# Performance work log

Hardware: AMD Instinct MI355X
Metric: run time of the kernel (lower is better)

## Reference

```python
import jax, jax.numpy as jnp
import numpy as np
import math

B, L, CIN = 16, 1024, 14
T = 256            # num_tokens
H = 2 * T          # S4 channel width
N = 32             # S4 state size (d_state)
E = 128            # embedding_dim
DEPTH = 6
BETA0, BETA1 = 1e-4, 2e-2


def conv1x1(W, b, x):
    # W: [O, C], b: [O], x: [B, C, L] -> [B, O, L]
    return jnp.einsum('oc,bcl->bol', W, x) + b[None, :, None]


def layernorm_c(x, g, b):
    # normalize over channel dim of [B, C, L]
    mu = jnp.mean(x, axis=1, keepdims=True)
    var = jnp.mean((x - mu) ** 2, axis=1, keepdims=True)
    return (x - mu) * jax.lax.rsqrt(var + 1e-5) * g[None, :, None] + b[None, :, None]


def s4d(u, log_dt, logA_re, A_im, C_re, C_im, D):
    # Standard S4D: diagonal SSM, ZOH-ish discretization, FFT depthwise conv.
    # u: [B, H, L]
    Lq = u.shape[-1]
    dt = jnp.exp(log_dt)                       # [H]
    A = -jnp.exp(logA_re) + 1j * A_im          # [H, N]
    dtA = A * dt[:, None]                      # [H, N]
    C = (C_re + 1j * C_im) * (jnp.exp(dtA) - 1.0) / A
    V = jnp.exp(dtA[:, :, None] * jnp.arange(Lq, dtype=jnp.float32))  # [H, N, L]
    K = 2.0 * jnp.einsum('hn,hnl->hl', C, V).real                    # [H, L]
    nfft = 2 * Lq
    y = jnp.fft.irfft(jnp.fft.rfft(u, n=nfft) * jnp.fft.rfft(K, n=nfft)[None], n=nfft)[..., :Lq]
    return y + D[None, :, None] * u


def setup_inputs() -> dict:
    key = jax.random.key(0)
    ks = iter(jax.random.split(key, 64))
    nrm = lambda shape, s=1.0: jax.random.normal(next(ks), shape, jnp.float32) * s
    inp = {}
    inp['x'] = nrm((B, L, CIN))
    inp['t'] = jax.random.uniform(next(ks), (B,), jnp.float32, 1e-3, 1.0)
    # diffusion embedding
    inp['gfp_W'] = nrm((E // 2,), 30.0)
    inp['emb_w1'] = nrm((E, E), E ** -0.5); inp['emb_b1'] = jnp.zeros((E,), jnp.float32)
    inp['emb_w2'] = nrm((E, E), E ** -0.5); inp['emb_b2'] = jnp.zeros((E,), jnp.float32)
    # top-level projections
    inp['in_w'] = nrm((T, CIN), CIN ** -0.5); inp['in_b'] = jnp.zeros((T,), jnp.float32)
    inp['out1_w'] = nrm((T, T), T ** -0.5); inp['out1_b'] = jnp.zeros((T,), jnp.float32)
    inp['out2_w'] = nrm((CIN, T), T ** -0.5); inp['out2_b'] = jnp.zeros((CIN,), jnp.float32)
    # per-block params (stacked over depth)
    inp['dp_w'] = nrm((DEPTH, T, E), E ** -0.5); inp['dp_b'] = jnp.zeros((DEPTH, T), jnp.float32)
    inp['ip_w'] = nrm((DEPTH, H, T), T ** -0.5); inp['ip_b'] = jnp.zeros((DEPTH, H), jnp.float32)
    inp['op_w'] = nrm((DEPTH, H, T), T ** -0.5); inp['op_b'] = jnp.zeros((DEPTH, H), jnp.float32)
    # S4D params: [DEPTH, 2, H, ...] (two S4 layers per block)
    lo, hi = math.log(1e-3), math.log(1e-1)
    inp['s4_log_dt'] = jax.random.uniform(next(ks), (DEPTH, 2, H), jnp.float32, lo, hi)
    inp['s4_logA_re'] = jnp.full((DEPTH, 2, H, N), math.log(0.5), jnp.float32)
    inp['s4_A_im'] = jnp.broadcast_to(math.pi * jnp.arange(N, dtype=jnp.float32), (DEPTH, 2, H, N)).copy()
    inp['s4_C_re'] = nrm((DEPTH, 2, H, N), 0.5 ** 0.5)
    inp['s4_C_im'] = nrm((DEPTH, 2, H, N), 0.5 ** 0.5)
    inp['s4_D'] = nrm((DEPTH, 2, H))
    inp['ln_g'] = jnp.ones((DEPTH, 2, H), jnp.float32)
    inp['ln_b'] = jnp.zeros((DEPTH, 2, H), jnp.float32)
    return inp


def reference(x, t, gfp_W, emb_w1, emb_b1, emb_w2, emb_b2, in_w, in_b,
              out1_w, out1_b, out2_w, out2_b, dp_w, dp_b, ip_w, ip_b,
              op_w, op_b, s4_log_dt, s4_logA_re, s4_A_im, s4_C_re, s4_C_im,
              s4_D, ln_g, ln_b):
    xt = jnp.swapaxes(x, -1, -2)  # [B, CIN, L]
    # Gaussian Fourier projection + MLP (SiLU)
    xp = t[:, None] * gfp_W[None, :] * (2.0 * math.pi)
    emb = jnp.concatenate([jnp.sin(xp), jnp.cos(xp)], axis=-1)        # [B, E]
    emb = jax.nn.silu(emb @ emb_w1.T + emb_b1)
    emb = jax.nn.silu(emb @ emb_w2.T + emb_b2)
    h = conv1x1(in_w, in_b, xt)                                       # [B, T, L]
    skip_sum = jnp.zeros_like(h)
    for d in range(DEPTH):
        y = h + (emb @ dp_w[d].T + dp_b[d])[:, :, None]
        y = conv1x1(ip_w[d], ip_b[d], y)                              # [B, H, L]
        y = s4d(y, s4_log_dt[d, 0], s4_logA_re[d, 0], s4_A_im[d, 0], s4_C_re[d, 0], s4_C_im[d, 0], s4_D[d, 0])
        y = layernorm_c(y, ln_g[d, 0], ln_b[d, 0])
        y = s4d(y, s4_log_dt[d, 1], s4_logA_re[d, 1], s4_A_im[d, 1], s4_C_re[d, 1], s4_C_im[d, 1], s4_D[d, 1])
        y = layernorm_c(y, ln_g[d, 1], ln_b[d, 1])
        gate, filt = jnp.split(y, 2, axis=1)
        y = jax.nn.sigmoid(gate) * jnp.tanh(filt)                     # [B, T, L]
        y = conv1x1(op_w[d], op_b[d], y)                              # [B, H, L]
        res, skip = jnp.split(y, 2, axis=1)
        h = (h + res) / math.sqrt(2.0)
        skip_sum = skip_sum + skip
    z = skip_sum / math.sqrt(float(DEPTH))
    z = jax.nn.relu(conv1x1(out1_w, out1_b, z))
    z = conv1x1(out2_w, out2_b, z)                                    # [B, CIN, L]
    beta = BETA0 + t * (BETA1 - BETA0)                                # linear schedule
    z = z / jnp.sqrt(beta)[:, None, None]
    return jnp.swapaxes(z, -1, -2)                                    # [B, L, CIN]
```

## Files before the change

kernel.cpp:

```cpp
#include <hip/hip_runtime.h>

#define BB     16
#define LLEN   1024
#define CINN   14
#define TSZ    256
#define HSZ    512
#define NST    32
#define ESZ    128
#define NDEPTH 6
#define QHN    (HSZ*NST)

#define RS2 0.70710678118654752f
#define IS6 0.40824829046386302f

typedef unsigned short u16;
typedef unsigned int   u32;
typedef _Float16 f16;
typedef __attribute__((ext_vector_type(2)))  _Float16 f16x2;
typedef __attribute__((ext_vector_type(4)))  _Float16 f16x4;
typedef __attribute__((ext_vector_type(8)))  _Float16 f16x8;
typedef __attribute__((ext_vector_type(16))) float    f32x16;

#define OFF_LAM   0u
#define OFF_C     393216u
#define OFF_LAMP  786432u
#define OFF_DPE16 1181696u
#define OFF_Y16   5388288u
#define OFF_HT    9582592u
#define OFF_GT    11679744u
#define OFF_ST    13776896u
#define OFF_ZT    15874048u
#define OFF_MEAN  17971200u
#define OFF_RSTD  17987584u
#define OFF_MATS  18003968u
#define WS_FLOATS 55752704u

#define MATS_PER_LAYER ((size_t)512*12288)

__global__ void consts_kernel(const float* __restrict__ log_dt, const float* __restrict__ logA,
                              const float* __restrict__ Aim,   const float* __restrict__ Cre,
                              const float* __restrict__ Cim,
                              float2* __restrict__ lam2, float2* __restrict__ C2,
                              float2* __restrict__ lamP){
  int gid = blockIdx.x*256 + threadIdx.x;
  int h = (gid>>5) & 511;
  int q = gid >> 14;
  float dt  = expf(log_dt[q*HSZ + h]);
  float are = -expf(logA[gid]);
  float aim = Aim[gid];
  float dre = are*dt, dim = aim*dt;
  float e   = expf(dre);
  float lre = e*cosf(dim), lim = e*sinf(dim);
  float nre = lre - 1.f, nim = lim;
  float invden = 1.f/(are*are + aim*aim);
  float tre = (nre*are + nim*aim)*invden;
  float tim = (nim*are - nre*aim)*invden;
  float cr = Cre[gid], ci = Cim[gid];
  float Cr = 2.f*(cr*tre - ci*tim);
  float Ci = 2.f*(cr*tim + ci*tre);
  lam2[gid] = make_float2(lre, lim);
  C2[gid]   = make_float2(Cr, Ci);
  float pr = lre, pi = lim;
#pragma unroll
  for (int i=0;i<6;i++){ float nr2 = pr*pr - pi*pi; pi = 2.f*pr*pi; pr = nr2; }
  lamP[gid] = make_float2(pr, pi);
}

__global__ __launch_bounds__(256) void build_mats(const float2* __restrict__ lam2d,
                                                  const float2* __restrict__ C2d,
                                                  const float* __restrict__ Dd,
                                                  f16* __restrict__ mats){
  __shared__ float Pre[65][33];
  __shared__ float Pim[65][33];
  __shared__ float Kk[64];
  int bid = blockIdx.x;
  int q   = bid >> 9;
  int h   = bid & 511;
  const float2* lp = lam2d + (size_t)q*QHN + h*NST;
  const float2* cp = C2d  + (size_t)q*QHN + h*NST;
  int tid = threadIdx.x;
  int n  = tid & 31;
  int pg = tid >> 5;
  {
    float2 l = lp[n];
    float ar=l.x, ai=l.y;
#pragma unroll
    for (int i=0;i<3;i++){ float t2 = ar*ar - ai*ai; ai = 2.f*ar*ai; ar = t2; }
    float br=1.f, bi=0.f;
    for (int i=0;i<pg;i++){ float t2 = br*ar - bi*ai; bi = br*ai + bi*ar; br = t2; }
    float pr=br, pi=bi;
#pragma unroll
    for (int i=0;i<8;i++){
      Pre[8*pg+i][n] = pr; Pim[8*pg+i][n] = pi;
      float t2 = pr*l.x - pi*l.y; pi = pr*l.y + pi*l.x; pr = t2;
    }
    if (pg == 7){ Pre[64][n] = pr; Pim[64][n] = pi; }
  }
  __syncthreads();
  if (tid < 64){
    float s = 0.f;
    for (int n2=0;n2<32;n2++){
      float2 c_ = cp[n2];
      s += c_.x*Pre[tid][n2] - c_.y*Pim[tid][n2];
    }
    Kk[tid] = s;
  }
  __syncthreads();
  float Kdiag = Kk[0] + Dd[q*HSZ + h];
  f16* base = mats + (size_t)bid*12288;
#pragma unroll
  for (int jj=0; jj<6; jj++){
    int job = jj*256 + tid;
    int mat = job >> 9;
    int rem = job & 511;
    int m = rem >> 3;
    int g = rem & 7;
    f16x8 vals;
    if (mat == 0){
#pragma unroll
      for (int j8=0;j8<8;j8++){
        int k = g*8 + j8;
        float v = (m > k) ? Kk[m-k] : ((m == k) ? Kdiag : 0.f);
        vals[j8] = (f16)v;
      }
    } else if (mat == 1){
      int n2 = m >> 1; int im = m & 1;
#pragma unroll
      for (int j8=0;j8<8;j8++){
        int k = g*8 + j8; int p = 63 - k;
        vals[j8] = (f16)(im ? Pim[p][n2] : Pre[p][n2]);
      }
    } else {
#pragma unroll
      for (int j8=0;j8<8;j8++){
        int k = g*8 + j8; int n2 = k >> 1;
        float2 c_ = cp[n2];
        float pr = Pre[m+1][n2], pi = Pim[m+1][n2];
        float re  = c_.x*pr - c_.y*pi;
        float imv = c_.x*pi + c_.y*pr;
        vals[j8] = (f16)((k & 1) ? -imv : re);
      }
    }
    *(f16x8*)(base + mat*4096 + (g*64 + m)*8) = vals;
  }
}

__global__ __launch_bounds__(256) void embdpe_kernel(const float* __restrict__ t, const float* __restrict__ gw,
                                                     const float* __restrict__ w1, const float* __restrict__ b1,
                                                     const float* __restrict__ w2, const float* __restrict__ b2,
                                                     const float* __restrict__ dw, const float* __restrict__ db,
                                                     f16* __restrict__ dpe16){
  __shared__ float e0[128], e1[128], e2[128];
  int bid = blockIdx.x;
  int d = bid >> 4, b = bid & 15;
  int tid = threadIdx.x;
  float tb = t[b];
  if (tid < 64){
    float xp = tb * gw[tid] * 6.283185307179586f;
    e0[tid]    = sinf(xp);
    e0[tid+64] = cosf(xp);
  }
  __syncthreads();
  if (tid < 128){
    float a = b1[tid];
    for (int i=0;i<128;i++) a = fmaf(e0[i], w1[tid*128+i], a);
    e1[tid] = a / (1.f + __expf(-a));
  }
  __syncthreads();
  if (tid < 128){
    float a2 = b2[tid];
    for (int i=0;i<128;i++) a2 = fmaf(e1[i], w2[tid*128+i], a2);
    e2[tid] = a2 / (1.f + __expf(-a2));
  }
  __syncthreads();
  int o = tid;
  const float* wp = dw + (size_t)(d*TSZ + o)*ESZ;
  float a = db[d*TSZ + o];
  for (int e=0;e<128;e++) a = fmaf(e2[e], wp[e], a);
  dpe16[(size_t)(d*BB + b)*TSZ + o] = (f16)a;
}

__global__ __launch_bounds__(256) void inproj_t_kernel(const float* __restrict__ x, const float* __restrict__ w,
                                                       const float* __restrict__ bias, f16* __restrict__ hT){
  __shared__ float ws[256*14];
  __shared__ float bs[256];
  __shared__ f16 TT[64*264];
  int tid = threadIdx.x;
#pragma unroll
  for (int c=0;c<14;c++) ws[tid*14+c] = w[tid*14+c];
  bs[tid] = bias[tid];
  __syncthreads();
  int b  = blockIdx.x >> 4;
  int l0 = (blockIdx.x & 15) * 64;
  int ll = tid & 63;
  int tq = tid >> 6;
  float xv[14];
  const float* xp = x + (size_t)(b*LLEN + l0 + ll)*CINN;
#pragma unroll
  for (int c=0;c<14;c++) xv[c] = xp[c];
  for (int tt=tq*64; tt<tq*64+64; tt++){
    float a = bs[tt];
#pragma unroll
    for (int c=0;c<14;c++) a = fmaf(ws[tt*14+c], xv[c], a);
    TT[ll*264 + tt] = (f16)a;
  }
  __syncthreads();
#pragma unroll
  for (int i=0;i<8;i++){
    int job = i*256 + tid;
    int l2 = job >> 5, g8 = (job & 31)*8;
    f16x8 hv = *(const f16x8*)(TT + l2*264 + g8);
    *(f16x8*)(hT + ((size_t)b*LLEN + l0 + l2)*TSZ + g8) = hv;
  }
}

template<int MODE>
__global__ __launch_bounds__(256) void gemm_k(const float* __restrict__ W, const float* __restrict__ bias,
                                              const f16* __restrict__ XT, const f16* __restrict__ dpeD,
                                              f16* __restrict__ Y16o,
                                              f16* __restrict__ hT16, f16* __restrict__ sT16, int first){
  __shared__ f16 sm[17408];
  f16* As = sm;
  f16* Bs = sm + 8192;
  int tid = threadIdx.x;
  int lane = tid & 63;
  int wv = tid >> 6;
  int n_blk = blockIdx.x * 128;
  int m_blk = blockIdx.y * 128;
  int bz = blockIdx.z;
  const f16* Xb = XT + (size_t)bz * (LLEN*TSZ);
  int wm = (wv & 1) * 64;
  int wn = (wv >> 1) * 64;

  f32x16 acc[2][2];
#pragma unroll
  for (int mi=0;mi<2;mi++)
#pragma unroll
    for (int ni=0;ni<2;ni++)
#pragma unroll
      for (int r=0;r<16;r++) acc[mi][ni][r] = 0.f;

  for (int kt=0; kt<4; kt++){
    int k0 = kt*64;
#pragma unroll
    for (int i=0;i<4;i++){
      int job = i*256 + tid;
      int m = job >> 3, gk = job & 7;
      const float* wp = W + (size_t)(m_blk + m)*TSZ + k0 + gk*8;
      float4 u0 = *(const float4*)wp;
      float4 u1 = *(const float4*)(wp+4);
      f16x8 hv;
      hv[0]=(f16)u0.x; hv[1]=(f16)u0.y; hv[2]=(f16)u0.z; hv[3]=(f16)u0.w;
      hv[4]=(f16)u1.x; hv[5]=(f16)u1.y; hv[6]=(f16)u1.z; hv[7]=(f16)u1.w;
      int P = m*8 + (gk ^ (m & 7));
      *(f16x8*)(As + P*8) = hv;
    }
#pragma unroll
    for (int i=0;i<4;i++){
      int job = i*256 + tid;
      int n = job >> 3, gk = job & 7;
      f16x8 hv = *(const f16x8*)(Xb + (size_t)(n_blk + n)*TSZ + k0 + gk*8);
      if (MODE==0){
        f16x8 dv = *(const f16x8*)(dpeD + bz*TSZ + k0 + gk*8);
#pragma unroll
        for (int e=0;e<8;e++) hv[e] = hv[e] + dv[e];
      }
      if (MODE==2){
#pragma unroll
        for (int e=0;e<8;e++) hv[e] = hv[e] * (f16)IS6;
      }
      int P = n*8 + (gk ^ (n & 7));
      *(f16x8*)(Bs + P*8) = hv;
    }
    __syncthreads();
#pragma unroll
    for (int ks=0; ks<4; ks++){
      int q = lane >> 5;
      int gk = ks*2 + q;
      f16x8 af[2], bf[2];
#pragma unroll
      for (int mi=0; mi<2; mi++){
        int m = wm + mi*32 + (lane & 31);
        af[mi] = *(const f16x8*)(As + (m*8 + (gk ^ (m&7)))*8);
      }
#pragma unroll
      for (int ni=0; ni<2; ni++){
        int n = wn + ni*32 + (lane & 31);
        bf[ni] = *(const f16x8*)(Bs + (n*8 + (gk ^ (n&7)))*8);
      }
#pragma unroll
      for (int mi=0; mi<2; mi++)
#pragma unroll
        for (int ni=0; ni<2; ni++)
          acc[mi][ni] = __builtin_amdgcn_mfma_f32_32x32x16_f16(af[mi], bf[ni], acc[mi][ni], 0, 0, 0);
    }
    __syncthreads();
  }

  int q = lane >> 5;
  if (MODE == 0){
#pragma unroll
    for (int mi=0;mi<2;mi++)
#pragma unroll
      for (int ni=0;ni<2;ni++){
        int col = n_blk + wn + ni*32 + (lane & 31);
#pragma unroll
        for (int r=0;r<16;r++){
          int row = m_blk + wm + mi*32 + (r&3) + 8*(r>>2) + 4*q;
          float v = acc[mi][ni][r] + bias[row];
          Y16o[((size_t)bz*HSZ + row)*LLEN + col] = (f16)v;
        }
      }
  } else if (MODE == 2){
#pragma unroll
    for (int mi=0;mi<2;mi++)
#pragma unroll
      for (int ni=0;ni<2;ni++){
        int col_l = wn + ni*32 + (lane & 31);
#pragma unroll
        for (int r=0;r<16;r++){
          int row_l = wm + mi*32 + (r&3) + 8*(r>>2) + 4*q;
          float v = fmaxf(acc[mi][ni][r] + bias[m_blk + row_l], 0.f);
          sm[col_l*136 + row_l] = (f16)v;
        }
      }
    __syncthreads();
#pragma unroll
    for (int i=0;i<8;i++){
      int job = i*256 + tid;
      int n = job >> 4, m8 = job & 15;
      f16x8 hv = *(const f16x8*)(sm + n*136 + m8*8);
      *(f16x8*)(Y16o + ((size_t)bz*LLEN + n_blk + n)*TSZ + m_blk + m8*8) = hv;
    }
  } else {
    int isRes = (blockIdx.y < 2);
    f16* dst = isRes ? hT16 : sT16;
    int mOff  = isRes ? m_blk : (m_blk - TSZ);
    int doLoad = isRes || !first;
    if (doLoad){
#pragma unroll
      for (int i=0;i<8;i++){
        int job = i*256 + tid;
        int n = job >> 4, m8 = job & 15;
        f16x8 hv = *(const f16x8*)(dst + ((size_t)bz*LLEN + n_blk + n)*TSZ + mOff + m8*8);
        *(f16x8*)(sm + n*136 + m8*8) = hv;
      }
      __syncthreads();
    }
#pragma unroll
    for (int mi=0;mi<2;mi++)
#pragma unroll
      for (int ni=0;ni<2;ni++){
        int col_l = wn + ni*32 + (lane & 31);
#pragma unroll
        for (int r=0;r<16;r++){
          int row_l = wm + mi*32 + (r&3) + 8*(r>>2) + 4*q;
          float v = acc[mi][ni][r] + bias[m_blk + row_l];
          if (isRes){
            float old = (float)sm[col_l*136 + row_l];
            sm[col_l*136 + row_l] = (f16)((old + v)*RS2);
          } else if (first){
            sm[col_l*136 + row_l] = (f16)v;
          } else {
            float old = (float)sm[col_l*136 + row_l];
            sm[col_l*136 + row_l] = (f16)(old + v);
          }
        }
      }
    __syncthreads();
#pragma unroll
    for (int i=0;i<8;i++){
      int job = i*256 + tid;
      int n = job >> 4, m8 = job & 15;
      f16x8 hv = *(const f16x8*)(sm + n*136 + m8*8);
      *(f16x8*)(dst + ((size_t)bz*LLEN + n_blk + n)*TSZ + mOff + m8*8) = hv;
    }
  }
}

template<int LN>
__global__ __launch_bounds__(128) void s4_mfma(const f16* __restrict__ matsq,
                                               const float2* __restrict__ lamPq,
                                               const f16* u, f16* y,
                                               const float* __restrict__ meanp,
                                               const float* __restrict__ rstdp,
                                               const float* __restrict__ gp,
                                               const float* __restrict__ btp){
  __shared__ f16 Ubuf[64*72];
  __shared__ f16 ZSbuf[64*72];

  int tid  = threadIdx.x;
  int w    = tid >> 6;
  int lane = tid & 63;
  int q    = lane >> 5;
  int colL = lane & 31;
  int h  = blockIdx.x & 511;
  int bq = blockIdx.x >> 9;
  int b0 = bq*4;

  float gv = 0.f, bv = 0.f;
  if (LN){ gv = gp[h]; bv = btp[h]; }

  const f16* matT = matsq + (size_t)h*12288;
  const f16* matV = matT + 4096;
  const f16* matE = matT + 8192;

#pragma unroll
  for (int i=0;i<4;i++){
    int fidx = i*64 + lane;
    int row = fidx >> 7;
    int l   = (fidx & 127)*8;
    int b   = b0 + 2*w + row;
    f16x8 hv = *(const f16x8*)(u + ((size_t)b*HSZ + h)*LLEN + l);
    if (LN){
      float4 m0 = *(const float4*)(meanp + b*LLEN + l);
      float4 m1 = *(const float4*)(meanp + b*LLEN + l + 4);
      float4 r0 = *(const float4*)(rstdp + b*LLEN + l);
      float4 r1 = *(const float4*)(rstdp + b*LLEN + l + 4);
      float mm[8] = {m0.x,m0.y,m0.z,m0.w,m1.x,m1.y,m1.z,m1.w};
      float rr[8] = {r0.x,r0.y,r0.z,r0.w,r1.x,r1.y,r1.z,r1.w};
#pragma unroll
      for (int e=0;e<8;e++)
        hv[e] = (f16)(((float)hv[e] - mm[e])*rr[e]*gv + bv);
    }
    int col = (2*w + row)*16 + (l >> 6);
    *(f16x8*)(Ubuf + col*72 + (l & 63)) = hv;
  }
  __syncthreads();

  int strip = w*32;

  {
    f32x16 zacc[2];
#pragma unroll
    for (int mt=0;mt<2;mt++)
#pragma unroll
      for (int r=0;r<16;r++) zacc[mt][r] = 0.f;
#pragma unroll
    for (int kt=0; kt<4; kt++){
      int kg = kt*2 + q;
      f16x8 bfrag = *(const f16x8*)(Ubuf + (strip+colL)*72 + kg*8);
#pragma unroll
      for (int mt=0; mt<2; mt++){
        f16x8 afrag = *(const f16x8*)(matV + ((size_t)(kg*64 + mt*32 + colL))*8);
        zacc[mt] = __builtin_amdgcn_mfma_f32_32x32x16_f16(afrag, bfrag, zacc[mt], 0, 0, 0);
      }
    }
#pragma unroll
    for (int mt=0;mt<2;mt++)
#pragma unroll
      for (int rg=0;rg<4;rg++){
        int st0 = mt*32 + rg*8 + q*4;
        f16x4 zp;
        zp[0]=(f16)zacc[mt][rg*4+0]; zp[1]=(f16)zacc[mt][rg*4+1];
        zp[2]=(f16)zacc[mt][rg*4+2]; zp[3]=(f16)zacc[mt][rg*4+3];
        *(f16x4*)(ZSbuf + (strip+colL)*72 + st0) = zp;
      }
  }
  __syncthreads();

  {
    int n  = lane & 31;
    int colb = (2*w + (lane>>5))*16;
    float2 l64 = lamPq[h*NST + n];
    float Sre = 0.f, Sim = 0.f;
#pragma unroll
    for (int c=0;c<16;c++){
      f16* p = ZSbuf + (colb + c)*72 + 2*n;
      f16x2 z2 = *(f16x2*)p;
      f16x2 sp_; sp_[0] = (f16)Sre; sp_[1] = (f16)Sim;
      *(f16x2*)p = sp_;
      float nr = fmaf(l64.x, Sre, fmaf(-l64.y, Sim, (float)z2[0]));
      float ni = fmaf(l64.x, Sim, fmaf( l64.y, Sre, (float)z2[1]));
      Sre = nr; Sim = ni;
    }
  }
  __syncthreads();

  f32x16 yacc[2];
#pragma unroll
  for (int mt=0;mt<2;mt++)
#pragma unroll
    for (int r=0;r<16;r++) yacc[mt][r] = 0.f;
#pragma unroll
  for (int kt=0; kt<4; kt++){
    int kg = kt*2 + q;
    f16x8 bu = *(const f16x8*)(Ubuf  + (strip+colL)*72 + kg*8);
    f16x8 bs = *(const f16x8*)(ZSbuf + (strip+colL)*72 + kg*8);
#pragma unroll
    for (int mt=0; mt<2; mt++){
      f16x8 aT = *(const f16x8*)(matT + ((size_t)(kg*64 + mt*32 + colL))*8);
      yacc[mt] = __builtin_amdgcn_mfma_f32_32x32x16_f16(aT, bu, yacc[mt], 0, 0, 0);
    }
#pragma unroll
    for (int mt=0; mt<2; mt++){
      f16x8 aE = *(const f16x8*)(matE + ((size_t)(kg*64 + mt*32 + colL))*8);
      yacc[mt] = __builtin_amdgcn_mfma_f32_32x32x16_f16(aE, bs, yacc[mt], 0, 0, 0);
    }
  }
  __syncthreads();

#pragma unroll
  for (int mt=0;mt<2;mt++)
#pragma unroll
    for (int rg=0;rg<4;rg++){
      int j0 = mt*32 + rg*8 + q*4;
      f16x4 yv;
      yv[0]=(f16)yacc[mt][rg*4+0]; yv[1]=(f16)yacc[mt][rg*4+1];
      yv[2]=(f16)yacc[mt][rg*4+2]; yv[3]=(f16)yacc[mt][rg*4+3];
      *(f16x4*)(ZSbuf + (strip+colL)*72 + j0) = yv;
    }
  __syncthreads();
#pragma unroll
  for (int i=0;i<4;i++){
    int fidx = i*64 + lane;
    int row = fidx >> 7;
    int l   = (fidx & 127)*8;
    int b   = b0 + 2*w + row;
    int col = (2*w + row)*16 + (l >> 6);
    f16x8 hv = *(const f16x8*)(ZSbuf + col*72 + (l & 63));
    *(f16x8*)(y + ((size_t)b*HSZ + h)*LLEN + l) = hv;
  }
}

__global__ __launch_bounds__(256) void ln_stats(const f16* __restrict__ in,
                                                float* __restrict__ mean, float* __restrict__ rstd){
  __shared__ float rs[4][32];
  __shared__ float rq[4][32];
  int tid = threadIdx.x;
  int lg = tid & 3;
  int hb = tid >> 2;
  int w  = tid >> 6;
  int b  = blockIdx.x >> 5;
  int l0 = (blockIdx.x & 31) << 5;
  float s8[8], q8[8];
#pragma unroll
  for (int j=0;j<8;j++){ s8[j]=0.f; q8[j]=0.f; }
  const f16* basep = in + (size_t)(b*HSZ)*LLEN + l0 + lg*8;
#pragma unroll
  for (int i=0;i<8;i++){
    int h = hb + 64*i;
    f16x8 hv = *(const f16x8*)(basep + (size_t)h*LLEN);
#pragma unroll
    for (int j=0;j<8;j++){
      float v = (float)hv[j];
      s8[j] += v; q8[j] = fmaf(v,v,q8[j]);
    }
  }
#pragma unroll
  for (int d=4; d<64; d<<=1){
#pragma unroll
    for (int j=0;j<8;j++){
      s8[j] += __shfl_xor(s8[j], (unsigned)d);
      q8[j] += __shfl_xor(q8[j], (unsigned)d);
    }
  }
  if (((tid>>2) & 15) == 0){
#pragma unroll
    for (int j=0;j<8;j++){
      rs[w][lg*8+j] = s8[j];
      rq[w][lg*8+j] = q8[j];
    }
  }
  __syncthreads();
  if (tid < 32){
    float S = rs[0][tid]+rs[1][tid]+rs[2][tid]+rs[3][tid];
    float Q = rq[0][tid]+rq[1][tid]+rq[2][tid]+rq[3][tid];
    float mn = S * (1.f/HSZ);
    float var = Q * (1.f/HSZ) - mn*mn;
    mean[b*LLEN + l0 + tid] = mn;
    rstd[b*LLEN + l0 + tid] = rsqrtf(var + 1e-5f);
  }
}

__global__ __launch_bounds__(256) void ln_gate_kernel(const f16* __restrict__ in, f16* __restrict__ gT,
                                                      const float* __restrict__ g, const float* __restrict__ bt){
  __shared__ float rs[4][32];
  __shared__ float rq[4][32];
  __shared__ float mbuf[32], rbuf[32];
  __shared__ f16 gbuf[32*264];
  int tid = threadIdx.x;
  int lg = tid & 3;
  int w  = tid >> 6;
  int b  = blockIdx.x >> 5;
  int l0 = (blockIdx.x & 31) << 5;
  {
    int hb = tid >> 2;
    float s8[8], q8[8];
#pragma unroll
    for (int j=0;j<8;j++){ s8[j]=0.f; q8[j]=0.f; }
    const f16* basep = in + (size_t)(b*HSZ)*LLEN + l0 + lg*8;
#pragma unroll
    for (int i=0;i<8;i++){
      int h = hb + 64*i;
      f16x8 hv = *(const f16x8*)(basep + (size_t)h*LLEN);
#pragma unroll
      for (int j=0;j<8;j++){
        float v = (float)hv[j];
        s8[j] += v; q8[j] = fmaf(v,v,q8[j]);
      }
    }
#pragma unroll
    for (int d=4; d<64; d<<=1){
#pragma unroll
      for (int j=0;j<8;j++){
        s8[j] += __shfl_xor(s8[j], (unsigned)d);
        q8[j] += __shfl_xor(q8[j], (unsigned)d);
      }
    }
    if (((tid>>2) & 15) == 0){
#pragma unroll
      for (int j=0;j<8;j++){
        rs[w][lg*8+j] = s8[j];
        rq[w][lg*8+j] = q8[j];
      }
    }
  }
  __syncthreads();
  if (tid < 32){
    float S = rs[0][tid]+rs[1][tid]+rs[2][tid]+rs[3][tid];
    float Q = rq[0][tid]+rq[1][tid]+rq[2][tid]+rq[3][tid];
    float mn = S * (1.f/HSZ);
    float var = Q * (1.f/HSZ) - mn*mn;
    mbuf[tid] = mn;
    rbuf[tid] = rsqrtf(var + 1e-5f);
  }
  __syncthreads();
  {
    int tq = tid >> 2;
    float mloc[8], rloc[8];
#pragma unroll
    for (int j=0;j<8;j++){ mloc[j]=mbuf[lg*8+j]; rloc[j]=rbuf[lg*8+j]; }
    const f16* basep = in + (size_t)(b*HSZ)*LLEN + l0 + lg*8;
#pragma unroll
    for (int i=0;i<4;i++){
      int t = tq + 64*i;
      f16x8 av = *(const f16x8*)(basep + (size_t)t*LLEN);
      f16x8 fv = *(const f16x8*)(basep + (size_t)(t+256)*LLEN);
      float ga = g[t], ba = bt[t], gf = g[t+256], bf2 = bt[t+256];
#pragma unroll
      for (int j=0;j<8;j++){
        float a = ((float)av[j] - mloc[j])*rloc[j]*ga + ba;
        float f = ((float)fv[j] - mloc[j])*rloc[j]*gf + bf2;
        float sg = 1.f/(1.f+__expf(-a));
        float th = 1.f - 2.f/(__expf(2.f*f)+1.f);
        gbuf[(lg*8+j)*264 + t] = (f16)(sg*th);
      }
    }
  }
  __syncthreads();
#pragma unroll
  for (int i=0;i<4;i++){
    int job = i*256 + tid;
    int ll = job >> 5, g8 = (job & 31)*8;
    f16x8 hv = *(const f16x8*)(gbuf + ll*264 + g8);
    *(f16x8*)(gT + ((size_t)b*LLEN + l0 + ll)*TSZ + g8) = hv;
  }
}

__global__ __launch_bounds__(256) void out2_kernel(const float* __restrict__ w2, const float* __restrict__ b2,
                                                   const float* __restrict__ t, const f16* __restrict__ zT,
                                                   float* __restrict__ outp){
  __shared__ f16 zt[64*264];
  __shared__ float wsm[14*256];
  __shared__ float part[64][4][16];
  __shared__ float bs[14];
  int tid = threadIdx.x;
#pragma unroll
  for (int c=0;c<14;c++) wsm[c*256+tid] = w2[c*256+tid];
  if (tid < 14) bs[tid] = b2[tid];
  int b = blockIdx.x >> 4;
  int l0 = (blockIdx.x & 15) * 64;
#pragma unroll
  for (int i=0;i<8;i++){
    int job = i*256 + tid;
    int ll = job >> 5, g8 = (job & 31)*8;
    f16x8 hv = *(const f16x8*)(zT + ((size_t)b*LLEN + l0 + ll)*TSZ + g8);
    *(f16x8*)(zt + ll*264 + g8) = hv;
  }
  __syncthreads();
  int l = tid >> 2;
  int g = tid & 3;
  float acc[14];
#pragma unroll
  for (int c=0;c<14;c++) acc[c]=0.f;
  for (int k=0;k<64;k++){
    float zv = (float)zt[l*264 + g*64 + k];
#pragma unroll
    for (int c=0;c<14;c++) acc[c] = fmaf(wsm[c*256 + g*64 + k], zv, acc[c]);
  }
#pragma unroll
  for (int c=0;c<14;c++) part[l][g][c] = acc[c];
  __syncthreads();
  if (g == 0){
    float tb = t[b];
    float scale = rsqrtf(1e-4f + tb*(2e-2f - 1e-4f));
    float* op = outp + (size_t)(b*LLEN + l0 + l)*CINN;
#pragma unroll
    for (int c=0;c<14;c++)
      op[c] = (part[l][0][c]+part[l][1][c]+part[l][2][c]+part[l][3][c] + bs[c])*scale;
  }
}

extern "C" void kernel_launch(void* const* d_in, const int* in_sizes, int n_in,
                              void* d_out, int out_size, void* d_ws, size_t ws_size,
                              hipStream_t stream) {
  (void)in_sizes; (void)n_in; (void)out_size;
  if (ws_size < (size_t)WS_FLOATS * 4) return;

  const float* x      = (const float*)d_in[0];
  const float* t      = (const float*)d_in[1];
  const float* gfpW   = (const float*)d_in[2];
  const float* ew1    = (const float*)d_in[3];
  const float* eb1    = (const float*)d_in[4];
  const float* ew2    = (const float*)d_in[5];
  const float* eb2    = (const float*)d_in[6];
  const float* in_w   = (const float*)d_in[7];
  const float* in_b   = (const float*)d_in[8];
  const float* out1_w = (const float*)d_in[9];
  const float* out1_b = (const float*)d_in[10];
  const float* out2_w = (const float*)d_in[11];
  const float* out2_b = (const float*)d_in[12];
  const float* dp_w   = (const float*)d_in[13];
  const float* dp_b   = (const float*)d_in[14];
  const float* ip_w   = (const float*)d_in[15];
  const float* ip_b   = (const float*)d_in[16];
  const float* op_w   = (const float*)d_in[17];
  const float* op_b   = (const float*)d_in[18];
  const float* log_dt = (const float*)d_in[19];
  const float* logA   = (const float*)d_in[20];
  const float* Aim    = (const float*)d_in[21];
  const float* Cre    = (const float*)d_in[22];
  const float* Cim    = (const float*)d_in[23];
  const float* s4D    = (const float*)d_in[24];
  const float* ln_g   = (const float*)d_in[25];
  const float* ln_b   = (const float*)d_in[26];
  float* out = (float*)d_out;
  float* ws = (float*)d_ws;

  float2* lam2  = (float2*)(ws + OFF_LAM);
  float2* C2v   = (float2*)(ws + OFF_C);
  float2* lamP  = (float2*)(ws + OFF_LAMP);
  f16*   dpe16 = (f16*)(ws + OFF_DPE16);
  f16*   y16   = (f16*)(ws + OFF_Y16);
  f16*   hT16  = (f16*)(ws + OFF_HT);
  f16*   gT16  = (f16*)(ws + OFF_GT);
  f16*   sT16  = (f16*)(ws + OFF_ST);
  f16*   zT16  = (f16*)(ws + OFF_ZT);
  float* meanb = ws + OFF_MEAN;
  float* rstdb = ws + OFF_RSTD;
  f16*   mats  = (f16*)(ws + OFF_MATS);

  consts_kernel<<<768,256,0,stream>>>(log_dt, logA, Aim, Cre, Cim, lam2, C2v, lamP);
  build_mats<<<6144,256,0,stream>>>(lam2, C2v, s4D, mats);
  embdpe_kernel<<<NDEPTH*BB,256,0,stream>>>(t, gfpW, ew1, eb1, ew2, eb2, dp_w, dp_b, dpe16);
  inproj_t_kernel<<<256,256,0,stream>>>(x, in_w, in_b, hT16);

  for (int d=0; d<NDEPTH; d++){
    int q0 = d*2, q1 = d*2+1;
    gemm_k<0><<<dim3(8,4,16),256,0,stream>>>(ip_w + (size_t)d*HSZ*TSZ, ip_b + d*HSZ,
                                             hT16, dpe16 + (size_t)d*BB*TSZ,
                                             y16, nullptr, nullptr, 0);
    s4_mfma<0><<<2048,128,0,stream>>>(mats + (size_t)q0*MATS_PER_LAYER, lamP + (size_t)q0*QHN,
                                      y16, y16, nullptr, nullptr, nullptr, nullptr);
    ln_stats<<<512,256,0,stream>>>(y16, meanb, rstdb);
    s4_mfma<1><<<2048,128,0,stream>>>(mats + (size_t)q1*MATS_PER_LAYER, lamP + (size_t)q1*QHN,
                                      y16, y16, meanb, rstdb, ln_g + q0*HSZ, ln_b + q0*HSZ);
    ln_gate_kernel<<<512,256,0,stream>>>(y16, gT16, ln_g + q1*HSZ, ln_b + q1*HSZ);
    gemm_k<1><<<dim3(8,4,16),256,0,stream>>>(op_w + (size_t)d*HSZ*TSZ, op_b + d*HSZ,
                                             gT16, nullptr, nullptr, hT16, sT16, (d==0)?1:0);
  }
  gemm_k<2><<<dim3(8,2,16),256,0,stream>>>(out1_w, out1_b, sT16, nullptr,
                                           zT16, nullptr, nullptr, 0);
  out2_kernel<<<256,256,0,stream>>>(out2_w, out2_b, t, zT16, out);
}
```

Measured before the change: 707.5 us.

## Pre-swizzle fp16 weights and activations so GEMMs load directly to LDS

A prep kernel converts the in/out projection and out1 weights to fp16 once, in a pre-swizzled tiled layout. Activations hT/gT are also stored in that swizzled layout, which lets gemm_k stage both operands with global_load_lds and no register conversion. The diffusion-embedding add is folded into a per-batch bias (W·dpe + b), so the per-element add in the GEMM load path goes away. The consts and build kernels are fused, and the embedding and in-projection kernels are merged, which cuts launches but leaves the 6 bias-folding blocks doing serial work.

```diff
diff --git a/kernel.cpp b/kernel.cpp
--- a/kernel.cpp
+++ b/kernel.cpp
@@ -21,10 +21,11 @@
 typedef __attribute__((ext_vector_type(8)))  _Float16 f16x8;
 typedef __attribute__((ext_vector_type(16))) float    f32x16;
 
-#define OFF_LAM   0u
-#define OFF_C     393216u
+#define OFF_WIP   0u
+#define OFF_WOP   393216u
 #define OFF_LAMP  786432u
-#define OFF_DPE16 1181696u
+#define OFF_WO1   1181696u
+#define OFF_BB    1214464u
 #define OFF_Y16   5388288u
 #define OFF_HT    9582592u
 #define OFF_GT    11679744u
@@ -37,52 +38,61 @@
 
 #define MATS_PER_LAYER ((size_t)512*12288)
 
-__global__ void consts_kernel(const float* __restrict__ log_dt, const float* __restrict__ logA,
-                              const float* __restrict__ Aim,   const float* __restrict__ Cre,
-                              const float* __restrict__ Cim,
-                              float2* __restrict__ lam2, float2* __restrict__ C2,
-                              float2* __restrict__ lamP){
-  int gid = blockIdx.x*256 + threadIdx.x;
-  int h = (gid>>5) & 511;
-  int q = gid >> 14;
-  float dt  = expf(log_dt[q*HSZ + h]);
-  float are = -expf(logA[gid]);
-  float aim = Aim[gid];
-  float dre = are*dt, dim = aim*dt;
-  float e   = expf(dre);
-  float lre = e*cosf(dim), lim = e*sinf(dim);
-  float nre = lre - 1.f, nim = lim;
-  float invden = 1.f/(are*are + aim*aim);
-  float tre = (nre*are + nim*aim)*invden;
-  float tim = (nim*are - nre*aim)*invden;
-  float cr = Cre[gid], ci = Cim[gid];
-  float Cr = 2.f*(cr*tre - ci*tim);
-  float Ci = 2.f*(cr*tim + ci*tre);
-  lam2[gid] = make_float2(lre, lim);
-  C2[gid]   = make_float2(Cr, Ci);
-  float pr = lre, pi = lim;
-#pragma unroll
-  for (int i=0;i<6;i++){ float nr2 = pr*pr - pi*pi; pi = 2.f*pr*pi; pr = nr2; }
-  lamP[gid] = make_float2(pr, pi);
-}
-
-__global__ __launch_bounds__(256) void build_mats(const float2* __restrict__ lam2d,
-                                                  const float2* __restrict__ C2d,
-                                                  const float* __restrict__ Dd,
-                                                  f16* __restrict__ mats){
+__device__ __forceinline__ void gload_lds16(const void* g, void* l){
+  __builtin_amdgcn_global_load_lds(
+      (const __attribute__((address_space(1))) unsigned int*)g,
+      (__attribute__((address_space(3))) unsigned int*)(unsigned int)(unsigned long long)l,
+      16, 0, 0);
+}
+
+__device__ __forceinline__ size_t swz_idx(int b, int l, int g){
+  return ((((size_t)b*4 + (g>>3))*1024 + l)*8 + ((g&7) ^ (l&7)))*8;
+}
+
+__global__ __launch_bounds__(256) void build_kernel(const float* __restrict__ log_dt,
+                                                    const float* __restrict__ logA,
+                                                    const float* __restrict__ Aim,
+                                                    const float* __restrict__ Cre,
+                                                    const float* __restrict__ Cim,
+                                                    const float* __restrict__ Dd,
+                                                    float2* __restrict__ lamP,
+                                                    f16* __restrict__ mats){
   __shared__ float Pre[65][33];
   __shared__ float Pim[65][33];
   __shared__ float Kk[64];
+  __shared__ float Kpart[4][64];
+  __shared__ float2 Lm[32];
+  __shared__ float2 Cc[32];
   int bid = blockIdx.x;
   int q   = bid >> 9;
   int h   = bid & 511;
-  const float2* lp = lam2d + (size_t)q*QHN + h*NST;
-  const float2* cp = C2d  + (size_t)q*QHN + h*NST;
   int tid = threadIdx.x;
+  if (tid < 32){
+    int n = tid;
+    int gid = q*QHN + h*NST + n;
+    float dt  = expf(log_dt[q*HSZ + h]);
+    float are = -expf(logA[gid]);
+    float aim = Aim[gid];
+    float dre = are*dt, dim = aim*dt;
+    float e   = expf(dre);
+    float lre = e*cosf(dim), lim = e*sinf(dim);
+    float nre = lre - 1.f, nim = lim;
+    float invden = 1.f/(are*are + aim*aim);
+    float tre = (nre*are + nim*aim)*invden;
+    float tim = (nim*are - nre*aim)*invden;
+    float cr = Cre[gid], ci = Cim[gid];
+    Lm[n] = make_float2(lre, lim);
+    Cc[n] = make_float2(2.f*(cr*tre - ci*tim), 2.f*(cr*tim + ci*tre));
+    float pr = lre, pi = lim;
+#pragma unroll
+    for (int i=0;i<6;i++){ float t2 = pr*pr - pi*pi; pi = 2.f*pr*pi; pr = t2; }
+    lamP[gid] = make_float2(pr, pi);
+  }
+  __syncthreads();
   int n  = tid & 31;
   int pg = tid >> 5;
   {
-    float2 l = lp[n];
+    float2 l = Lm[n];
     float ar=l.x, ai=l.y;
 #pragma unroll
     for (int i=0;i<3;i++){ float t2 = ar*ar - ai*ai; ai = 2.f*ar*ai; ar = t2; }
@@ -97,14 +107,18 @@
     if (pg == 7){ Pre[64][n] = pr; Pim[64][n] = pi; }
   }
   __syncthreads();
-  if (tid < 64){
+  {
+    int m = tid & 63, p2 = tid >> 6;
     float s = 0.f;
-    for (int n2=0;n2<32;n2++){
-      float2 c_ = cp[n2];
-      s += c_.x*Pre[tid][n2] - c_.y*Pim[tid][n2];
-    }
-    Kk[tid] = s;
-  }
+#pragma unroll
+    for (int n2=p2*8; n2<p2*8+8; n2++){
+      float2 c_ = Cc[n2];
+      s += c_.x*Pre[m][n2] - c_.y*Pim[m][n2];
+    }
+    Kpart[p2][m] = s;
+  }
+  __syncthreads();
+  if (tid < 64) Kk[tid] = Kpart[0][tid]+Kpart[1][tid]+Kpart[2][tid]+Kpart[3][tid];
   __syncthreads();
   float Kdiag = Kk[0] + Dd[q*HSZ + h];
   f16* base = mats + (size_t)bid*12288;
@@ -134,7 +148,7 @@
 #pragma unroll
       for (int j8=0;j8<8;j8++){
         int k = g*8 + j8; int n2 = k >> 1;
-        float2 c_ = cp[n2];
+        float2 c_ = Cc[n2];
         float pr = Pre[m+1][n2], pi = Pim[m+1][n2];
         float re  = c_.x*pr - c_.y*pi;
         float imv = c_.x*pi + c_.y*pr;
@@ -145,81 +159,140 @@
   }
 }
 
-__global__ __launch_bounds__(256) void embdpe_kernel(const float* __restrict__ t, const float* __restrict__ gw,
-                                                     const float* __restrict__ w1, const float* __restrict__ b1,
-                                                     const float* __restrict__ w2, const float* __restrict__ b2,
-                                                     const float* __restrict__ dw, const float* __restrict__ db,
-                                                     f16* __restrict__ dpe16){
-  __shared__ float e0[128], e1[128], e2[128];
+__global__ __launch_bounds__(256) void prep2(const float* __restrict__ tv, const float* __restrict__ gw,
+                                             const float* __restrict__ w1, const float* __restrict__ b1,
+                                             const float* __restrict__ w2, const float* __restrict__ b2,
+                                             const float* __restrict__ dw, const float* __restrict__ db,
+                                             const float* __restrict__ ipw, const float* __restrict__ ipb,
+                                             const float* __restrict__ x,  const float* __restrict__ inw,
+                                             const float* __restrict__ inb,
+                                             const float* __restrict__ opw, const float* __restrict__ o1w,
+                                             f16* __restrict__ WfIP, f16* __restrict__ WfOP,
+                                             f16* __restrict__ WfO1, float* __restrict__ bbp,
+                                             f16* __restrict__ hT){
+  __shared__ __align__(16) char SMEM[49152];
   int bid = blockIdx.x;
-  int d = bid >> 4, b = bid & 15;
   int tid = threadIdx.x;
-  float tb = t[b];
-  if (tid < 64){
-    float xp = tb * gw[tid] * 6.283185307179586f;
-    e0[tid]    = sinf(xp);
-    e0[tid+64] = cosf(xp);
-  }
-  __syncthreads();
-  if (tid < 128){
-    float a = b1[tid];
-    for (int i=0;i<128;i++) a = fmaf(e0[i], w1[tid*128+i], a);
-    e1[tid] = a / (1.f + __expf(-a));
-  }
-  __syncthreads();
-  if (tid < 128){
-    float a2 = b2[tid];
-    for (int i=0;i<128;i++) a2 = fmaf(e1[i], w2[tid*128+i], a2);
-    e2[tid] = a2 / (1.f + __expf(-a2));
-  }
-  __syncthreads();
-  int o = tid;
-  const float* wp = dw + (size_t)(d*TSZ + o)*ESZ;
-  float a = db[d*TSZ + o];
-  for (int e=0;e<128;e++) a = fmaf(e2[e], wp[e], a);
-  dpe16[(size_t)(d*BB + b)*TSZ + o] = (f16)a;
-}
-
-__global__ __launch_bounds__(256) void inproj_t_kernel(const float* __restrict__ x, const float* __restrict__ w,
-                                                       const float* __restrict__ bias, f16* __restrict__ hT){
-  __shared__ float ws[256*14];
-  __shared__ float bs[256];
-  __shared__ f16 TT[64*264];
-  int tid = threadIdx.x;
-#pragma unroll
-  for (int c=0;c<14;c++) ws[tid*14+c] = w[tid*14+c];
-  bs[tid] = bias[tid];
-  __syncthreads();
-  int b  = blockIdx.x >> 4;
-  int l0 = (blockIdx.x & 15) * 64;
-  int ll = tid & 63;
-  int tq = tid >> 6;
-  float xv[14];
-  const float* xp = x + (size_t)(b*LLEN + l0 + ll)*CINN;
-#pragma unroll
-  for (int c=0;c<14;c++) xv[c] = xp[c];
-  for (int tt=tq*64; tt<tq*64+64; tt++){
-    float a = bs[tt];
-#pragma unroll
-    for (int c=0;c<14;c++) a = fmaf(ws[tt*14+c], xv[c], a);
-    TT[ll*264 + tt] = (f16)a;
-  }
-  __syncthreads();
-#pragma unroll
-  for (int i=0;i<8;i++){
-    int job = i*256 + tid;
-    int l2 = job >> 5, g8 = (job & 31)*8;
-    f16x8 hv = *(const f16x8*)(TT + l2*264 + g8);
-    *(f16x8*)(hT + ((size_t)b*LLEN + l0 + l2)*TSZ + g8) = hv;
+  if (bid < 6){
+    float* E0  = (float*)SMEM;
+    float* E1  = (float*)(SMEM + 8192);
+    float* DPE = (float*)(SMEM + 16384);
+    float* ROW = (float*)(SMEM + 32832);
+    int d = bid;
+#pragma unroll
+    for (int i=0;i<8;i++){
+      int job = i*256 + tid; int b = job>>7, e = job&127;
+      float xp = tv[b] * gw[e&63] * 6.283185307179586f;
+      E0[b*128+e] = (e < 64) ? sinf(xp) : cosf(xp);
+    }
+    __syncthreads();
+#pragma unroll
+    for (int i=0;i<8;i++){
+      int job = i*256 + tid; int b = job>>7, o = job&127;
+      float a = b1[o]; const float* wr = w1 + o*128;
+      for (int e=0;e<128;e++) a = fmaf(E0[b*128+e], wr[e], a);
+      E1[b*128+o] = a / (1.f + __expf(-a));
+    }
+    __syncthreads();
+#pragma unroll
+    for (int i=0;i<8;i++){
+      int job = i*256 + tid; int b = job>>7, o = job&127;
+      float a = b2[o]; const float* wr = w2 + o*128;
+      for (int e=0;e<128;e++) a = fmaf(E1[b*128+e], wr[e], a);
+      E0[b*128+o] = a / (1.f + __expf(-a));
+    }
+    __syncthreads();
+#pragma unroll
+    for (int i=0;i<16;i++){
+      int job = i*256 + tid; int b = job>>8, o = job&255;
+      float a = db[d*256 + o]; const float* wr = dw + (size_t)(d*256 + o)*128;
+      for (int e=0;e<128;e++) a = fmaf(E0[b*128+e], wr[e], a);
+      DPE[b*257 + o] = a;
+    }
+    __syncthreads();
+    int b = tid >> 4, p = tid & 15;
+    for (int m0=0; m0<512; m0+=8){
+#pragma unroll
+      for (int i=0;i<8;i++) ROW[i*256+tid] = ipw[((size_t)d*512 + m0 + i)*256 + tid];
+      __syncthreads();
+#pragma unroll
+      for (int i=0;i<8;i++){
+        const float* rp = ROW + i*256 + p*16;
+        const float* dp2 = DPE + b*257 + p*16;
+        float s = 0.f;
+#pragma unroll
+        for (int j=0;j<16;j++) s = fmaf(rp[j], dp2[j], s);
+        s += __shfl_xor(s,1); s += __shfl_xor(s,2);
+        s += __shfl_xor(s,4); s += __shfl_xor(s,8);
+        if (p == 0) bbp[(size_t)(d*16 + b)*512 + m0 + i] = s + ipb[d*512 + m0 + i];
+      }
+      __syncthreads();
+    }
+  } else if (bid < 262){
+    float* ws  = (float*)SMEM;
+    float* bs2 = (float*)(SMEM + 14336);
+    f16*  TT   = (f16*)(SMEM + 15360);
+#pragma unroll
+    for (int c=0;c<14;c++) ws[tid*14+c] = inw[tid*14+c];
+    bs2[tid] = inb[tid];
+    __syncthreads();
+    int bb2 = bid - 6;
+    int b  = bb2 >> 4;
+    int l0 = (bb2 & 15) * 64;
+    int ll = tid & 63;
+    int tq = tid >> 6;
+    float xv[14];
+    const float* xp = x + (size_t)(b*LLEN + l0 + ll)*CINN;
+#pragma unroll
+    for (int c=0;c<14;c++) xv[c] = xp[c];
+    for (int tt=tq*64; tt<tq*64+64; tt++){
+      float a = bs2[tt];
+#pragma unroll
+      for (int c=0;c<14;c++) a = fmaf(ws[tt*14+c], xv[c], a);
+      TT[ll*264 + tt] = (f16)a;
+    }
+    __syncthreads();
+#pragma unroll
+    for (int i=0;i<8;i++){
+      int job = i*256 + tid;
+      int l2 = job >> 5, gi = job & 31;
+      f16x8 hv = *(const f16x8*)(TT + l2*264 + gi*8);
+      *(f16x8*)(hT + swz_idx(b, l0 + l2, gi)) = hv;
+    }
+  } else {
+    int gid = (bid - 262)*256 + tid;
+    const float* src; f16* dst; float scale = 1.f;
+    if (gid < 98304){
+      int d = gid >> 14, rem = gid & 16383, r = rem >> 5, g = rem & 31;
+      src = ipw + ((size_t)(d*512 + r))*256 + g*8;
+      dst = WfIP + (size_t)d*131072 + (((g>>3)*512 + r)*8 + ((g&7)^(r&7)))*8;
+    } else if (gid < 196608){
+      int g2 = gid - 98304;
+      int d = g2 >> 14, rem = g2 & 16383, r = rem >> 5, g = rem & 31;
+      src = opw + ((size_t)(d*512 + r))*256 + g*8;
+      dst = WfOP + (size_t)d*131072 + (((g>>3)*512 + r)*8 + ((g&7)^(r&7)))*8;
+    } else {
+      int g3 = gid - 196608;
+      int r = g3 >> 5, g = g3 & 31;
+      src = o1w + (size_t)r*256 + g*8;
+      dst = WfO1 + (((g>>3)*256 + r)*8 + ((g&7)^(r&7)))*8;
+      scale = IS6;
+    }
+    float4 u0 = *(const float4*)src;
+    float4 u1 = *(const float4*)(src+4);
+    f16x8 hv;
+    hv[0]=(f16)(u0.x*scale); hv[1]=(f16)(u0.y*scale); hv[2]=(f16)(u0.z*scale); hv[3]=(f16)(u0.w*scale);
+    hv[4]=(f16)(u1.x*scale); hv[5]=(f16)(u1.y*scale); hv[6]=(f16)(u1.z*scale); hv[7]=(f16)(u1.w*scale);
+    *(f16x8*)dst = hv;
   }
 }
 
 template<int MODE>
-__global__ __launch_bounds__(256) void gemm_k(const float* __restrict__ W, const float* __restrict__ bias,
-                                              const f16* __restrict__ XT, const f16* __restrict__ dpeD,
+__global__ __launch_bounds__(256) void gemm_k(const f16* __restrict__ Wf, const float* __restrict__ bias,
+                                              const f16* __restrict__ XT,
                                               f16* __restrict__ Y16o,
                                               f16* __restrict__ hT16, f16* __restrict__ sT16, int first){
-  __shared__ f16 sm[17408];
+  __shared__ __align__(16) f16 sm[17408];
   f16* As = sm;
   f16* Bs = sm + 8192;
   int tid = threadIdx.x;
@@ -228,7 +301,7 @@
   int n_blk = blockIdx.x * 128;
   int m_blk = blockIdx.y * 128;
   int bz = blockIdx.z;
-  const f16* Xb = XT + (size_t)bz * (LLEN*TSZ);
+  const int M = (MODE==2) ? 256 : 512;
   int wm = (wv & 1) * 64;
   int wn = (wv >> 1) * 64;
 
@@ -241,36 +314,12 @@
       for (int r=0;r<16;r++) acc[mi][ni][r] = 0.f;
 
   for (int kt=0; kt<4; kt++){
-    int k0 = kt*64;
+    const f16* asrc = Wf + ((size_t)kt*M + m_blk)*64 + tid*8;
+    const f16* bsrc = XT + ((size_t)(bz*4 + kt)*1024 + n_blk)*64 + tid*8;
 #pragma unroll
     for (int i=0;i<4;i++){
-      int job = i*256 + tid;
-      int m = job >> 3, gk = job & 7;
-      const float* wp = W + (size_t)(m_blk + m)*TSZ + k0 + gk*8;
-      float4 u0 = *(const float4*)wp;
-      float4 u1 = *(const float4*)(wp+4);
-      f16x8 hv;
-      hv[0]=(f16)u0.x; hv[1]=(f16)u0.y; hv[2]=(f16)u0.z; hv[3]=(f16)u0.w;
-      hv[4]=(f16)u1.x; hv[5]=(f16)u1.y; hv[6]=(f16)u1.z; hv[7]=(f16)u1.w;
-      int P = m*8 + (gk ^ (m & 7));
-      *(f16x8*)(As + P*8) = hv;
-    }
-#pragma unroll
-    for (int i=0;i<4;i++){
-      int job = i*256 + tid;
-      int n = job >> 3, gk = job & 7;
-      f16x8 hv = *(const f16x8*)(Xb + (size_t)(n_blk + n)*TSZ + k0 + gk*8);
-      if (MODE==0){
-        f16x8 dv = *(const f16x8*)(dpeD + bz*TSZ + k0 + gk*8);
-#pragma unroll
-        for (int e=0;e<8;e++) hv[e] = hv[e] + dv[e];
-      }
-      if (MODE==2){
-#pragma unroll
-        for (int e=0;e<8;e++) hv[e] = hv[e] * (f16)IS6;
-      }
-      int P = n*8 + (gk ^ (n & 7));
-      *(f16x8*)(Bs + P*8) = hv;
+      gload_lds16(asrc + i*2048, As + (i*256 + wv*64)*8);
+      gload_lds16(bsrc + i*2048, Bs + (i*256 + wv*64)*8);
     }
     __syncthreads();
 #pragma unroll
@@ -307,7 +356,7 @@
 #pragma unroll
         for (int r=0;r<16;r++){
           int row = m_blk + wm + mi*32 + (r&3) + 8*(r>>2) + 4*q;
-          float v = acc[mi][ni][r] + bias[row];
+          float v = acc[mi][ni][r] + bias[bz*HSZ + row];
           Y16o[((size_t)bz*HSZ + row)*LLEN + col] = (f16)v;
         }
       }
@@ -335,14 +384,14 @@
   } else {
     int isRes = (blockIdx.y < 2);
     f16* dst = isRes ? hT16 : sT16;
-    int mOff  = isRes ? m_blk : (m_blk - TSZ);
+    int gbase = isRes ? (m_blk >> 3) : ((m_blk - TSZ) >> 3);
     int doLoad = isRes || !first;
     if (doLoad){
 #pragma unroll
       for (int i=0;i<8;i++){
         int job = i*256 + tid;
         int n = job >> 4, m8 = job & 15;
-        f16x8 hv = *(const f16x8*)(dst + ((size_t)bz*LLEN + n_blk + n)*TSZ + mOff + m8*8);
+        f16x8 hv = *(const f16x8*)(dst + swz_idx(bz, n_blk + n, gbase + m8));
         *(f16x8*)(sm + n*136 + m8*8) = hv;
       }
       __syncthreads();
@@ -373,7 +422,7 @@
       int job = i*256 + tid;
       int n = job >> 4, m8 = job & 15;
       f16x8 hv = *(const f16x8*)(sm + n*136 + m8*8);
-      *(f16x8*)(dst + ((size_t)bz*LLEN + n_blk + n)*TSZ + mOff + m8*8) = hv;
+      *(f16x8*)(dst + swz_idx(bz, n_blk + n, gbase + m8)) = hv;
     }
   }
 }
@@ -652,9 +701,9 @@
 #pragma unroll
   for (int i=0;i<4;i++){
     int job = i*256 + tid;
-    int ll = job >> 5, g8 = (job & 31)*8;
-    f16x8 hv = *(const f16x8*)(gbuf + ll*264 + g8);
-    *(f16x8*)(gT + ((size_t)b*LLEN + l0 + ll)*TSZ + g8) = hv;
+    int ll = job >> 5, gi = job & 31;
+    f16x8 hv = *(const f16x8*)(gbuf + ll*264 + gi*8);
+    *(f16x8*)(gT + swz_idx(b, l0 + ll, gi)) = hv;
   }
 }
 
@@ -738,39 +787,38 @@
   float* out = (float*)d_out;
   float* ws = (float*)d_ws;
 
-  float2* lam2  = (float2*)(ws + OFF_LAM);
-  float2* C2v   = (float2*)(ws + OFF_C);
-  float2* lamP  = (float2*)(ws + OFF_LAMP);
-  f16*   dpe16 = (f16*)(ws + OFF_DPE16);
-  f16*   y16   = (f16*)(ws + OFF_Y16);
-  f16*   hT16  = (f16*)(ws + OFF_HT);
-  f16*   gT16  = (f16*)(ws + OFF_GT);
-  f16*   sT16  = (f16*)(ws + OFF_ST);
-  f16*   zT16  = (f16*)(ws + OFF_ZT);
-  float* meanb = ws + OFF_MEAN;
-  float* rstdb = ws + OFF_RSTD;
-  f16*   mats  = (f16*)(ws + OFF_MATS);
-
-  consts_kernel<<<768,256,0,stream>>>(log_dt, logA, Aim, Cre, Cim, lam2, C2v, lamP);
-  build_mats<<<6144,256,0,stream>>>(lam2, C2v, s4D, mats);
-  embdpe_kernel<<<NDEPTH*BB,256,0,stream>>>(t, gfpW, ew1, eb1, ew2, eb2, dp_w, dp_b, dpe16);
-  inproj_t_kernel<<<256,256,0,stream>>>(x, in_w, in_b, hT16);
+  f16*    WfIP = (f16*)(ws + OFF_WIP);
+  f16*    WfOP = (f16*)(ws + OFF_WOP);
+  float2* lamP = (float2*)(ws + OFF_LAMP);
+  f16*    WfO1 = (f16*)(ws + OFF_WO1);
+  float*  bbp  = ws + OFF_BB;
+  f16*    y16  = (f16*)(ws + OFF_Y16);
+  f16*    hT16 = (f16*)(ws + OFF_HT);
+  f16*    gT16 = (f16*)(ws + OFF_GT);
+  f16*    sT16 = (f16*)(ws + OFF_ST);
+  f16*    zT16 = (f16*)(ws + OFF_ZT);
+  float*  meanb = ws + OFF_MEAN;
+  float*  rstdb = ws + OFF_RSTD;
+  f16*    mats = (f16*)(ws + OFF_MATS);
+
+  build_kernel<<<6144,256,0,stream>>>(log_dt, logA, Aim, Cre, Cim, s4D, lamP, mats);
+  prep2<<<1062,256,0,stream>>>(t, gfpW, ew1, eb1, ew2, eb2, dp_w, dp_b, ip_w, ip_b,
+                               x, in_w, in_b, op_w, out1_w,
+                               WfIP, WfOP, WfO1, bbp, hT16);
 
   for (int d=0; d<NDEPTH; d++){
     int q0 = d*2, q1 = d*2+1;
-    gemm_k<0><<<dim3(8,4,16),256,0,stream>>>(ip_w + (size_t)d*HSZ*TSZ, ip_b + d*HSZ,
-                                             hT16, dpe16 + (size_t)d*BB*TSZ,
-                                             y16, nullptr, nullptr, 0);
+    gemm_k<0><<<dim3(8,4,16),256,0,stream>>>(WfIP + (size_t)d*131072, bbp + (size_t)d*BB*HSZ,
+                                             hT16, y16, nullptr, nullptr, 0);
     s4_mfma<0><<<2048,128,0,stream>>>(mats + (size_t)q0*MATS_PER_LAYER, lamP + (size_t)q0*QHN,
                                       y16, y16, nullptr, nullptr, nullptr, nullptr);
     ln_stats<<<512,256,0,stream>>>(y16, meanb, rstdb);
     s4_mfma<1><<<2048,128,0,stream>>>(mats + (size_t)q1*MATS_PER_LAYER, lamP + (size_t)q1*QHN,
                                       y16, y16, meanb, rstdb, ln_g + q0*HSZ, ln_b + q0*HSZ);
     ln_gate_kernel<<<512,256,0,stream>>>(y16, gT16, ln_g + q1*HSZ, ln_b + q1*HSZ);
-    gemm_k<1><<<dim3(8,4,16),256,0,stream>>>(op_w + (size_t)d*HSZ*TSZ, op_b + d*HSZ,
-                                             gT16, nullptr, nullptr, hT16, sT16, (d==0)?1:0);
-  }
-  gemm_k<2><<<dim3(8,2,16),256,0,stream>>>(out1_w, out1_b, sT16, nullptr,
-                                           zT16, nullptr, nullptr, 0);
+    gemm_k<1><<<dim3(8,4,16),256,0,stream>>>(WfOP + (size_t)d*131072, op_b + d*HSZ,
+                                             gT16, nullptr, hT16, sT16, (d==0)?1:0);
+  }
+  gemm_k<2><<<dim3(8,2,16),256,0,stream>>>(WfO1, out1_b, sT16, zT16, nullptr, nullptr, 0);
   out2_kernel<<<256,256,0,stream>>>(out2_w, out2_b, t, zT16, out);
 }
```

Measured after the change: 1.260 ms. 78.1% more time.
